# Kernel optimization log

Measured on AMD Instinct MI355X. Metric: run time of the kernel, lower is better.

## Reference

```python
import jax, jax.numpy as jnp
import numpy as np

H = 16          # head_count
D = 1024        # model_dim
DH = D // H     # dim_per_head


def setup_inputs() -> dict:
    key = jax.random.key(0)
    ks = jax.random.split(key, 12)
    B, S = 4, 2048
    s = 1.0 / np.sqrt(D)
    return {
        "key": jax.random.normal(ks[0], (B, S, D), jnp.float32),
        "value": jax.random.normal(ks[1], (B, S, D), jnp.float32),
        "query": jax.random.normal(ks[2], (B, S, D), jnp.float32),
        "Wk": jax.random.normal(ks[3], (D, D), jnp.float32) * s,
        "bk": jax.random.normal(ks[4], (D,), jnp.float32) * 0.01,
        "Wv": jax.random.normal(ks[5], (D, D), jnp.float32) * s,
        "bv": jax.random.normal(ks[6], (D,), jnp.float32) * 0.01,
        "Wq": jax.random.normal(ks[7], (D, D), jnp.float32) * s,
        "bq": jax.random.normal(ks[8], (D,), jnp.float32) * 0.01,
        "Wo": jax.random.normal(ks[9], (D, D), jnp.float32) * s,
        "bo": jax.random.normal(ks[10], (D,), jnp.float32) * 0.01,
    }


def _split_heads(x):
    # [B, S, D] -> [B, H, S, DH]
    B, S, _ = x.shape
    return x.reshape(B, S, H, DH).transpose(0, 2, 1, 3)


def reference(key, value, query, Wk, bk, Wv, bv, Wq, bq, Wo, bo):
    B, Sq, _ = query.shape
    Sk = key.shape[1]
    k_up = _split_heads(key @ Wk + bk)      # [B,H,Sk,DH]
    v_up = _split_heads(value @ Wv + bv)    # [B,H,Sk,DH]
    q_up = _split_heads(query @ Wq + bq) / jnp.sqrt(jnp.asarray(DH, query.dtype))
    scores = jnp.einsum('bhqd,bhkd->bhqk', q_up, k_up)  # [B,H,Sq,Sk]
    attn = jax.nn.softmax(scores, axis=-1)
    # dropout p=0.0 -> identity
    ctx = jnp.einsum('bhqk,bhkd->bhqd', attn, v_up)      # [B,H,Sq,DH]
    ctx = ctx.transpose(0, 2, 1, 3).reshape(B, Sq, D)    # combine heads
    output = ctx @ Wo + bo
    top_attn = attn[:, 0, :, :]
    return output, top_attn
```

## Files before the change

kernel.cpp:

```cpp
#include <hip/hip_runtime.h>
#include <stdint.h>

typedef __bf16 bf16_t;
typedef __bf16 bf16x8 __attribute__((ext_vector_type(8)));
typedef float f32x4 __attribute__((ext_vector_type(4)));
typedef uint32_t u32x4 __attribute__((ext_vector_type(4)));

#define D_MODEL 1024
#define NH      16
#define DH      64
#define SEQ     2048
#define BATCH   4
#define MROWS   (BATCH * SEQ)

#define VCOL(d, c) ((c) ^ ((((d) >> 3) & 3) << 4))

__device__ __forceinline__ void gll16(const void* g, void* l) {
    __builtin_amdgcn_global_load_lds(
        (const __attribute__((address_space(1))) void*)g,
        (__attribute__((address_space(3))) void*)l, 16, 0, 0);
}

__global__ void transpose_w(const float* __restrict__ W0, const float* __restrict__ W1,
                            const float* __restrict__ W2, const float* __restrict__ W3,
                            bf16_t* __restrict__ out) {
    __shared__ bf16_t tile[32][33];
    const int z = blockIdx.z;
    const float* src = (z == 0) ? W0 : (z == 1) ? W1 : (z == 2) ? W2 : W3;
    bf16_t* dst = out + (size_t)z * (D_MODEL * D_MODEL);
    const int bx = blockIdx.x * 32, by = blockIdx.y * 32;
    const int tx = threadIdx.x, ty = threadIdx.y;
#pragma unroll
    for (int i = 0; i < 4; ++i)
        tile[ty + i * 8][tx] = (bf16_t)src[(size_t)(by + ty + i * 8) * D_MODEL + bx + tx];
    __syncthreads();
#pragma unroll
    for (int i = 0; i < 4; ++i)
        dst[(size_t)(bx + ty + i * 8) * D_MODEL + by + tx] = tile[tx][ty + i * 8];
}

__global__ __launch_bounds__(256) void cast_bf16(const float* __restrict__ in,
                                                 bf16_t* __restrict__ out, int n8) {
    const int i = blockIdx.x * 256 + threadIdx.x;
    if (i < n8) {
        const float4 x = ((const float4*)in)[i * 2];
        const float4 y = ((const float4*)in)[i * 2 + 1];
        bf16x8 t;
        t[0] = (bf16_t)x.x; t[1] = (bf16_t)x.y; t[2] = (bf16_t)x.z; t[3] = (bf16_t)x.w;
        t[4] = (bf16_t)y.x; t[5] = (bf16_t)y.y; t[6] = (bf16_t)y.z; t[7] = (bf16_t)y.w;
        ((bf16x8*)out)[i] = t;
    }
}

template<int OUT_MODE>
__global__ __launch_bounds__(256) void proj_gemm(const bf16_t* __restrict__ A,
                                                 const bf16_t* __restrict__ Wt,
                                                 const float* __restrict__ bias,
                                                 void* __restrict__ C_,
                                                 float scale) {
    __shared__ __align__(16) bf16_t As[128 * 32];
    __shared__ __align__(16) bf16_t Bs[128 * 32];
    const int tid  = threadIdx.x;
    const int lane = tid & 63;
    const int w    = tid >> 6;
    const int wrow = (w >> 1) * 64;
    const int wcol = (w & 1) * 64;
    const int m0 = blockIdx.y * 128;
    const int n0 = blockIdx.x * 128;
    const int l15  = lane & 15;
    const int quad = lane >> 4;
    const int srow = w * 32 + (lane >> 2);
    const int scol = (lane & 3) * 8;

    f32x4 acc[4][4];
#pragma unroll
    for (int i = 0; i < 4; ++i)
#pragma unroll
        for (int j = 0; j < 4; ++j)
#pragma unroll
            for (int r = 0; r < 4; ++r) acc[i][j][r] = 0.0f;

    for (int kt = 0; kt < 32; ++kt) {
        const int k0 = kt * 32;
#pragma unroll
        for (int j = 0; j < 2; ++j) {
            gll16(A  + (size_t)(m0 + srow + j * 16) * D_MODEL + k0 + scol,
                  &As[(w * 32 + j * 16) * 32]);
            gll16(Wt + (size_t)(n0 + srow + j * 16) * D_MODEL + k0 + scol,
                  &Bs[(w * 32 + j * 16) * 32]);
        }
        __syncthreads();
        bf16x8 af[4], bf[4];
#pragma unroll
        for (int mi = 0; mi < 4; ++mi)
            af[mi] = *(const bf16x8*)&As[(wrow + mi * 16 + l15) * 32 + quad * 8];
#pragma unroll
        for (int ni = 0; ni < 4; ++ni)
            bf[ni] = *(const bf16x8*)&Bs[(wcol + ni * 16 + l15) * 32 + quad * 8];
#pragma unroll
        for (int mi = 0; mi < 4; ++mi)
#pragma unroll
            for (int ni = 0; ni < 4; ++ni)
                acc[mi][ni] = __builtin_amdgcn_mfma_f32_16x16x32_bf16(af[mi], bf[ni], acc[mi][ni], 0, 0, 0);
        __syncthreads();
    }

#pragma unroll
    for (int ni = 0; ni < 4; ++ni) {
        const int col = n0 + wcol + ni * 16 + l15;
        const float bc = bias[col];
#pragma unroll
        for (int mi = 0; mi < 4; ++mi) {
#pragma unroll
            for (int r = 0; r < 4; ++r) {
                const int row = m0 + wrow + mi * 16 + quad * 4 + r;
                const float v = (acc[mi][ni][r] + bc) * scale;
                if (OUT_MODE == 1) {
                    ((float*)C_)[(size_t)row * D_MODEL + col] = v;
                } else if (OUT_MODE == 0) {
                    ((bf16_t*)C_)[(size_t)row * D_MODEL + col] = (bf16_t)v;
                } else {
                    const int bb = row >> 11, ss = row & 2047;
                    const int hh = col >> 6,  dd = col & 63;
                    ((bf16_t*)C_)[((size_t)(bb * 16 + hh) * 64 + dd) * 2048 + ss] = (bf16_t)v;
                }
            }
        }
    }
}

__device__ __forceinline__ uint32_t pk2(float a, float b) {
    union { bf16_t h[2]; uint32_t u; } x;
    x.h[0] = (bf16_t)a; x.h[1] = (bf16_t)b;
    return x.u;
}

__global__ __launch_bounds__(256) void flash_attn(const bf16_t* __restrict__ Qu,
                                                  const bf16_t* __restrict__ Ku,
                                                  const bf16_t* __restrict__ Vt_g,
                                                  bf16_t* __restrict__ ctx) {
    const int qt = blockIdx.x;
    const int bh = blockIdx.y;
    const int b = bh >> 4, h = bh & 15;
    const int tid  = threadIdx.x;
    const int lane = tid & 63;
    const int w    = tid >> 6;
    const int l15  = lane & 15;
    const int quad = lane >> 4;

    __shared__ __align__(16) bf16_t Ks[64][72];
    __shared__ __align__(16) bf16_t Vs[64][72];

    const size_t base_qk = (size_t)b * SEQ * D_MODEL + (size_t)h * DH;
    const size_t base_v  = (size_t)bh * DH * SEQ;
    const int qrow0 = qt * 64 + w * 16;

    bf16x8 qf[2];
#pragma unroll
    for (int ks = 0; ks < 2; ++ks)
        qf[ks] = *(const bf16x8*)(Qu + base_qk + (size_t)(qrow0 + l15) * D_MODEL + ks * 32 + quad * 8);

    const int srow = tid >> 2;
    const int sc0  = (tid & 3) * 16;
    const bf16_t* kg = Ku   + base_qk + (size_t)srow * D_MODEL + sc0;
    const bf16_t* vg = Vt_g + base_v  + (size_t)srow * SEQ + sc0;

    bf16x8 kp0, kp1, vp0, vp1;
#define LOAD_TILE(KB)                                                    \
    do {                                                                 \
        kp0 = *(const bf16x8*)(kg + (size_t)(KB) * D_MODEL);             \
        kp1 = *(const bf16x8*)(kg + (size_t)(KB) * D_MODEL + 8);         \
        vp0 = *(const bf16x8*)(vg + (KB));                               \
        vp1 = *(const bf16x8*)(vg + (KB) + 8);                           \
    } while (0)
#define WRITE_TILE()                                                     \
    do {                                                                 \
        *(bf16x8*)&Ks[srow][VCOL(srow, sc0)]     = kp0;                  \
        *(bf16x8*)&Ks[srow][VCOL(srow, sc0 + 8)] = kp1;                  \
        *(bf16x8*)&Vs[srow][VCOL(srow, sc0)]     = vp0;                  \
        *(bf16x8*)&Vs[srow][VCOL(srow, sc0 + 8)] = vp1;                  \
    } while (0)

    float m_q = -__builtin_inff();
    float l_q = 0.0f;
    f32x4 cacc[4];
#pragma unroll
    for (int ds = 0; ds < 4; ++ds)
#pragma unroll
        for (int r = 0; r < 4; ++r) cacc[ds][r] = 0.0f;

    LOAD_TILE(0);
    WRITE_TILE();

    for (int kt = 0; kt < 32; ++kt) {
        __syncthreads();
        if (kt + 1 < 32) LOAD_TILE((kt + 1) * 64);

        f32x4 s[4];
#pragma unroll
        for (int ki = 0; ki < 4; ++ki)
#pragma unroll
            for (int r = 0; r < 4; ++r) s[ki][r] = 0.0f;
#pragma unroll
        for (int ks = 0; ks < 2; ++ks)
#pragma unroll
            for (int ki = 0; ki < 4; ++ki) {
                const int kr = ki * 16 + l15;
                bf16x8 kf = *(const bf16x8*)&Ks[kr][VCOL(kr, ks * 32 + quad * 8)];
                s[ki] = __builtin_amdgcn_mfma_f32_16x16x32_bf16(kf, qf[ks], s[ki], 0, 0, 0);
            }

        float v = s[0][0];
#pragma unroll
        for (int ki = 0; ki < 4; ++ki)
#pragma unroll
            for (int r = 0; r < 4; ++r) v = fmaxf(v, s[ki][r]);
        v = fmaxf(v, __shfl_xor(v, 16));
        v = fmaxf(v, __shfl_xor(v, 32));
        const float mn  = fmaxf(m_q, v);
        const float alq = __expf(m_q - mn);
        m_q = mn;

        float t = 0.0f;
        uint32_t pk_[4][2];
#pragma unroll
        for (int ki = 0; ki < 4; ++ki) {
            const float p0 = __expf(s[ki][0] - mn);
            const float p1 = __expf(s[ki][1] - mn);
            const float p2 = __expf(s[ki][2] - mn);
            const float p3 = __expf(s[ki][3] - mn);
            t += (p0 + p1) + (p2 + p3);
            pk_[ki][0] = pk2(p0, p1);
            pk_[ki][1] = pk2(p2, p3);
        }
        t += __shfl_xor(t, 16);
        t += __shfl_xor(t, 32);
        l_q = l_q * alq + t;

        float al_c[4];
#pragma unroll
        for (int r = 0; r < 4; ++r) al_c[r] = __shfl(alq, quad * 4 + r, 16);
#pragma unroll
        for (int ds = 0; ds < 4; ++ds)
#pragma unroll
            for (int r = 0; r < 4; ++r) cacc[ds][r] *= al_c[r];

        const int srcA = l15 + ((quad & 1) << 5);
        const bool hi  = (quad & 2) != 0;
        bf16x8 af[2];
#pragma unroll
        for (int ks = 0; ks < 2; ++ks) {
            const uint32_t a0 = pk_[2 * ks][0],     a1 = pk_[2 * ks][1];
            const uint32_t b0 = pk_[2 * ks + 1][0], b1 = pk_[2 * ks + 1][1];
            union { u32x4 d; bf16x8 v8; } cv;
            const uint32_t xa = (uint32_t)__shfl((int)a0, srcA);
            const uint32_t xb = (uint32_t)__shfl((int)b0, srcA);
            cv.d.x = hi ? xb : xa;
            const uint32_t ya = (uint32_t)__shfl((int)a1, srcA);
            const uint32_t yb = (uint32_t)__shfl((int)b1, srcA);
            cv.d.y = hi ? yb : ya;
            const uint32_t za = (uint32_t)__shfl((int)a0, srcA + 16);
            const uint32_t zb = (uint32_t)__shfl((int)b0, srcA + 16);
            cv.d.z = hi ? zb : za;
            const uint32_t wa = (uint32_t)__shfl((int)a1, srcA + 16);
            const uint32_t wb = (uint32_t)__shfl((int)b1, srcA + 16);
            cv.d.w = hi ? wb : wa;
            af[ks] = cv.v8;
        }

#pragma unroll
        for (int ks = 0; ks < 2; ++ks)
#pragma unroll
            for (int ds = 0; ds < 4; ++ds) {
                const int vr = ds * 16 + l15;
                bf16x8 vf = *(const bf16x8*)&Vs[vr][VCOL(vr, ks * 32 + quad * 8)];
                cacc[ds] = __builtin_amdgcn_mfma_f32_16x16x32_bf16(af[ks], vf, cacc[ds], 0, 0, 0);
            }

        __syncthreads();
        if (kt + 1 < 32) WRITE_TILE();
    }

    float l_c[4];
#pragma unroll
    for (int r = 0; r < 4; ++r) l_c[r] = __shfl(l_q, quad * 4 + r, 16);
#pragma unroll
    for (int r = 0; r < 4; ++r) {
        const float rl = 1.0f / l_c[r];
        const int q = qrow0 + quad * 4 + r;
#pragma unroll
        for (int ds = 0; ds < 4; ++ds)
            ctx[(size_t)(b * SEQ + q) * D_MODEL + h * DH + ds * 16 + l15] = (bf16_t)(cacc[ds][r] * rl);
    }
#undef LOAD_TILE
#undef WRITE_TILE
}

__global__ __launch_bounds__(256) void attn_h0(const bf16_t* __restrict__ Qu,
                                               const bf16_t* __restrict__ Ku,
                                               float* __restrict__ out) {
    const int qt = blockIdx.x;
    const int b  = blockIdx.y;
    const int tid  = threadIdx.x;
    const int lane = tid & 63;
    const int w    = tid >> 6;
    const int l15  = lane & 15;
    const int quad = lane >> 4;

    const size_t base_b = (size_t)b * SEQ * D_MODEL;
    const int qrow0 = qt * 64 + w * 16;

    bf16x8 qf[2];
#pragma unroll
    for (int ks = 0; ks < 2; ++ks)
        qf[ks] = *(const bf16x8*)(Qu + base_b + (size_t)(qrow0 + l15) * D_MODEL + ks * 32 + quad * 8);

    float m_r[4], l_r[4];
#pragma unroll
    for (int r = 0; r < 4; ++r) { m_r[r] = -__builtin_inff(); l_r[r] = 0.0f; }

    for (int kt = 0; kt < 32; ++kt) {
        const int kb = kt * 64;
        f32x4 s[4];
#pragma unroll
        for (int ki = 0; ki < 4; ++ki)
#pragma unroll
            for (int r = 0; r < 4; ++r) s[ki][r] = 0.0f;
#pragma unroll
        for (int ks = 0; ks < 2; ++ks)
#pragma unroll
            for (int ki = 0; ki < 4; ++ki) {
                bf16x8 kf = *(const bf16x8*)(Ku + base_b + (size_t)(kb + ki * 16 + l15) * D_MODEL + ks * 32 + quad * 8);
                s[ki] = __builtin_amdgcn_mfma_f32_16x16x32_bf16(qf[ks], kf, s[ki], 0, 0, 0);
            }
#pragma unroll
        for (int r = 0; r < 4; ++r) {
            float v = fmaxf(fmaxf(s[0][r], s[1][r]), fmaxf(s[2][r], s[3][r]));
#pragma unroll
            for (int off = 1; off < 16; off <<= 1) v = fmaxf(v, __shfl_xor(v, off, 16));
            const float mn = fmaxf(m_r[r], v);
            const float al = __expf(m_r[r] - mn);
            m_r[r] = mn;
            float t = __expf(s[0][r] - mn) + __expf(s[1][r] - mn)
                    + __expf(s[2][r] - mn) + __expf(s[3][r] - mn);
#pragma unroll
            for (int off = 1; off < 16; off <<= 1) t += __shfl_xor(t, off, 16);
            l_r[r] = l_r[r] * al + t;
        }
    }
    float rl[4];
#pragma unroll
    for (int r = 0; r < 4; ++r) rl[r] = 1.0f / l_r[r];

    for (int kt = 0; kt < 32; ++kt) {
        const int kb = kt * 64;
        f32x4 s[4];
#pragma unroll
        for (int ki = 0; ki < 4; ++ki)
#pragma unroll
            for (int r = 0; r < 4; ++r) s[ki][r] = 0.0f;
#pragma unroll
        for (int ks = 0; ks < 2; ++ks)
#pragma unroll
            for (int ki = 0; ki < 4; ++ki) {
                bf16x8 kf = *(const bf16x8*)(Ku + base_b + (size_t)(kb + ki * 16 + l15) * D_MODEL + ks * 32 + quad * 8);
                s[ki] = __builtin_amdgcn_mfma_f32_16x16x32_bf16(qf[ks], kf, s[ki], 0, 0, 0);
            }
#pragma unroll
        for (int ki = 0; ki < 4; ++ki)
#pragma unroll
            for (int r = 0; r < 4; ++r) {
                const int q = qrow0 + quad * 4 + r;
                out[(size_t)(b * SEQ + q) * SEQ + kb + ki * 16 + l15] =
                    __expf(s[ki][r] - m_r[r]) * rl[r];
            }
    }
}

extern "C" void kernel_launch(void* const* d_in, const int* in_sizes, int n_in,
                              void* d_out, int out_size, void* d_ws, size_t ws_size,
                              hipStream_t stream) {
    const float* key   = (const float*)d_in[0];
    const float* value = (const float*)d_in[1];
    const float* query = (const float*)d_in[2];
    const float* Wk = (const float*)d_in[3];
    const float* bk = (const float*)d_in[4];
    const float* Wv = (const float*)d_in[5];
    const float* bv = (const float*)d_in[6];
    const float* Wq = (const float*)d_in[7];
    const float* bq = (const float*)d_in[8];
    const float* Wo = (const float*)d_in[9];
    const float* bo = (const float*)d_in[10];

    float* out_proj = (float*)d_out;
    float* out_attn = (float*)d_out + (size_t)MROWS * D_MODEL;

    char* ws = (char*)d_ws;
    bf16_t* Wt  = (bf16_t*)ws;
    bf16_t* Kup = (bf16_t*)(ws + (size_t) 8 * 1024 * 1024);
    bf16_t* Qup = (bf16_t*)(ws + (size_t)24 * 1024 * 1024);

    bf16_t* Vt_g = (bf16_t*)out_attn;
    bf16_t* ctx  = Vt_g + (size_t)MROWS * D_MODEL;
    bf16_t* C1   = (bf16_t*)((char*)out_attn + ((size_t)32 << 20));
    bf16_t* C2   = (bf16_t*)((char*)out_attn + ((size_t)48 << 20));

    const bf16_t* Wt_k = Wt;
    const bf16_t* Wt_v = Wt + 1 * D_MODEL * D_MODEL;
    const bf16_t* Wt_q = Wt + 2 * D_MODEL * D_MODEL;
    const bf16_t* Wt_o = Wt + 3 * D_MODEL * D_MODEL;

    const int n8 = MROWS * D_MODEL / 8;

    transpose_w<<<dim3(32, 32, 4), dim3(32, 8), 0, stream>>>(Wk, Wv, Wq, Wo, Wt);

    cast_bf16<<<dim3(4096), 256, 0, stream>>>(key,   C1, n8);
    cast_bf16<<<dim3(4096), 256, 0, stream>>>(value, C2, n8);

    proj_gemm<0><<<dim3(8, 64), 256, 0, stream>>>(C1, Wt_k, bk, Kup,  1.0f);
    cast_bf16<<<dim3(4096), 256, 0, stream>>>(query, C1, n8);
    proj_gemm<2><<<dim3(8, 64), 256, 0, stream>>>(C2, Wt_v, bv, Vt_g, 1.0f);
    proj_gemm<0><<<dim3(8, 64), 256, 0, stream>>>(C1, Wt_q, bq, Qup,  0.125f);

    flash_attn<<<dim3(32, 64), 256, 0, stream>>>(Qup, Kup, Vt_g, ctx);

    proj_gemm<1><<<dim3(8, 64), 256, 0, stream>>>(ctx, Wt_o, bo, out_proj, 1.0f);

    attn_h0<<<dim3(32, 4), 256, 0, stream>>>(Qup, Kup, out_attn);
}
```

Before: 584.3 us.

## Reuse flash softmax stats for head-0 attention, exp2 with lazy rescale, fused casts

flash_attn now writes the per-row max and inverse sum for head 0 to a workspace buffer. attn_h0 becomes a single-pass kernel tiled over key blocks (4096 blocks instead of 128), so it no longer recomputes the softmax statistics in a serial two-pass loop. The softmax uses a raw v_exp_f32 with log2e folded into the Q projection scale. Rescaling of the accumulator is skipped unless the running max grows by more than 8, which saves ALU work at a small accuracy cost. The three input casts are merged into one launch by giving the query its own buffer.

New measurement: 520.3 us. -11.0%, faster.

```diff
diff --git a/kernel.cpp b/kernel.cpp
--- a/kernel.cpp
+++ b/kernel.cpp
@@ -12,6 +12,10 @@
 #define SEQ     2048
 #define BATCH   4
 #define MROWS   (BATCH * SEQ)
+
+__device__ __forceinline__ float ex2(float x) {
+    float r; asm("v_exp_f32 %0, %1" : "=v"(r) : "v"(x)); return r;
+}
 
 #define VCOL(d, c) ((c) ^ ((((d) >> 3) & 3) << 4))
 
@@ -39,9 +43,16 @@
         dst[(size_t)(bx + ty + i * 8) * D_MODEL + by + tx] = tile[tx][ty + i * 8];
 }
 
-__global__ __launch_bounds__(256) void cast_bf16(const float* __restrict__ in,
-                                                 bf16_t* __restrict__ out, int n8) {
+__global__ __launch_bounds__(256) void cast3_bf16(const float* __restrict__ i0,
+                                                  const float* __restrict__ i1,
+                                                  const float* __restrict__ i2,
+                                                  bf16_t* __restrict__ o0,
+                                                  bf16_t* __restrict__ o1,
+                                                  bf16_t* __restrict__ o2, int n8) {
     const int i = blockIdx.x * 256 + threadIdx.x;
+    const int z = blockIdx.y;
+    const float* in  = (z == 0) ? i0 : (z == 1) ? i1 : i2;
+    bf16_t*      out = (z == 0) ? o0 : (z == 1) ? o1 : o2;
     if (i < n8) {
         const float4 x = ((const float4*)in)[i * 2];
         const float4 y = ((const float4*)in)[i * 2 + 1];
@@ -138,7 +149,9 @@
 __global__ __launch_bounds__(256) void flash_attn(const bf16_t* __restrict__ Qu,
                                                   const bf16_t* __restrict__ Ku,
                                                   const bf16_t* __restrict__ Vt_g,
-                                                  bf16_t* __restrict__ ctx) {
+                                                  bf16_t* __restrict__ ctx,
+                                                  float* __restrict__ Mb,
+                                                  float* __restrict__ Lb) {
     const int qt = blockIdx.x;
     const int bh = blockIdx.y;
     const int b = bh >> 4, h = bh & 15;
@@ -217,33 +230,36 @@
             for (int r = 0; r < 4; ++r) v = fmaxf(v, s[ki][r]);
         v = fmaxf(v, __shfl_xor(v, 16));
         v = fmaxf(v, __shfl_xor(v, 32));
-        const float mn  = fmaxf(m_q, v);
-        const float alq = __expf(m_q - mn);
-        m_q = mn;
+
+        if (!__all(v <= m_q + 8.0f)) {
+            const float mn  = fmaxf(m_q, v);
+            const float alq = ex2(m_q - mn);
+            m_q = mn;
+            l_q *= alq;
+            float al_c[4];
+#pragma unroll
+            for (int r = 0; r < 4; ++r) al_c[r] = __shfl(alq, quad * 4 + r, 16);
+#pragma unroll
+            for (int ds = 0; ds < 4; ++ds)
+#pragma unroll
+                for (int r = 0; r < 4; ++r) cacc[ds][r] *= al_c[r];
+        }
 
         float t = 0.0f;
         uint32_t pk_[4][2];
 #pragma unroll
         for (int ki = 0; ki < 4; ++ki) {
-            const float p0 = __expf(s[ki][0] - mn);
-            const float p1 = __expf(s[ki][1] - mn);
-            const float p2 = __expf(s[ki][2] - mn);
-            const float p3 = __expf(s[ki][3] - mn);
+            const float p0 = ex2(s[ki][0] - m_q);
+            const float p1 = ex2(s[ki][1] - m_q);
+            const float p2 = ex2(s[ki][2] - m_q);
+            const float p3 = ex2(s[ki][3] - m_q);
             t += (p0 + p1) + (p2 + p3);
             pk_[ki][0] = pk2(p0, p1);
             pk_[ki][1] = pk2(p2, p3);
         }
         t += __shfl_xor(t, 16);
         t += __shfl_xor(t, 32);
-        l_q = l_q * alq + t;
-
-        float al_c[4];
-#pragma unroll
-        for (int r = 0; r < 4; ++r) al_c[r] = __shfl(alq, quad * 4 + r, 16);
-#pragma unroll
-        for (int ds = 0; ds < 4; ++ds)
-#pragma unroll
-            for (int r = 0; r < 4; ++r) cacc[ds][r] *= al_c[r];
+        l_q += t;
 
         const int srcA = l15 + ((quad & 1) << 5);
         const bool hi  = (quad & 2) != 0;
@@ -281,6 +297,12 @@
         if (kt + 1 < 32) WRITE_TILE();
     }
 
+    if (h == 0 && quad == 0) {
+        const int q = b * SEQ + qrow0 + l15;
+        Mb[q] = m_q;
+        Lb[q] = 1.0f / l_q;
+    }
+
     float l_c[4];
 #pragma unroll
     for (int r = 0; r < 4; ++r) l_c[r] = __shfl(l_q, quad * 4 + r, 16);
@@ -298,9 +320,12 @@
 
 __global__ __launch_bounds__(256) void attn_h0(const bf16_t* __restrict__ Qu,
                                                const bf16_t* __restrict__ Ku,
+                                               const float* __restrict__ Mb,
+                                               const float* __restrict__ Lb,
                                                float* __restrict__ out) {
     const int qt = blockIdx.x;
-    const int b  = blockIdx.y;
+    const int ktile = blockIdx.y;
+    const int b  = blockIdx.z;
     const int tid  = threadIdx.x;
     const int lane = tid & 63;
     const int w    = tid >> 6;
@@ -309,72 +334,41 @@
 
     const size_t base_b = (size_t)b * SEQ * D_MODEL;
     const int qrow0 = qt * 64 + w * 16;
+    const int kb = ktile * 64;
 
     bf16x8 qf[2];
 #pragma unroll
     for (int ks = 0; ks < 2; ++ks)
         qf[ks] = *(const bf16x8*)(Qu + base_b + (size_t)(qrow0 + l15) * D_MODEL + ks * 32 + quad * 8);
 
-    float m_r[4], l_r[4];
-#pragma unroll
-    for (int r = 0; r < 4; ++r) { m_r[r] = -__builtin_inff(); l_r[r] = 0.0f; }
-
-    for (int kt = 0; kt < 32; ++kt) {
-        const int kb = kt * 64;
-        f32x4 s[4];
-#pragma unroll
-        for (int ki = 0; ki < 4; ++ki)
-#pragma unroll
-            for (int r = 0; r < 4; ++r) s[ki][r] = 0.0f;
-#pragma unroll
-        for (int ks = 0; ks < 2; ++ks)
-#pragma unroll
-            for (int ki = 0; ki < 4; ++ki) {
-                bf16x8 kf = *(const bf16x8*)(Ku + base_b + (size_t)(kb + ki * 16 + l15) * D_MODEL + ks * 32 + quad * 8);
-                s[ki] = __builtin_amdgcn_mfma_f32_16x16x32_bf16(qf[ks], kf, s[ki], 0, 0, 0);
-            }
+    f32x4 s[4];
+#pragma unroll
+    for (int ki = 0; ki < 4; ++ki)
+#pragma unroll
+        for (int r = 0; r < 4; ++r) s[ki][r] = 0.0f;
+#pragma unroll
+    for (int ks = 0; ks < 2; ++ks)
+#pragma unroll
+        for (int ki = 0; ki < 4; ++ki) {
+            bf16x8 kf = *(const bf16x8*)(Ku + base_b + (size_t)(kb + ki * 16 + l15) * D_MODEL + ks * 32 + quad * 8);
+            s[ki] = __builtin_amdgcn_mfma_f32_16x16x32_bf16(qf[ks], kf, s[ki], 0, 0, 0);
+        }
+
+    float m_v[4], rl_v[4];
+#pragma unroll
+    for (int r = 0; r < 4; ++r) {
+        const int q = b * SEQ + qrow0 + quad * 4 + r;
+        m_v[r]  = Mb[q];
+        rl_v[r] = Lb[q];
+    }
+#pragma unroll
+    for (int ki = 0; ki < 4; ++ki)
 #pragma unroll
         for (int r = 0; r < 4; ++r) {
-            float v = fmaxf(fmaxf(s[0][r], s[1][r]), fmaxf(s[2][r], s[3][r]));
-#pragma unroll
-            for (int off = 1; off < 16; off <<= 1) v = fmaxf(v, __shfl_xor(v, off, 16));
-            const float mn = fmaxf(m_r[r], v);
-            const float al = __expf(m_r[r] - mn);
-            m_r[r] = mn;
-            float t = __expf(s[0][r] - mn) + __expf(s[1][r] - mn)
-                    + __expf(s[2][r] - mn) + __expf(s[3][r] - mn);
-#pragma unroll
-            for (int off = 1; off < 16; off <<= 1) t += __shfl_xor(t, off, 16);
-            l_r[r] = l_r[r] * al + t;
-        }
-    }
-    float rl[4];
-#pragma unroll
-    for (int r = 0; r < 4; ++r) rl[r] = 1.0f / l_r[r];
-
-    for (int kt = 0; kt < 32; ++kt) {
-        const int kb = kt * 64;
-        f32x4 s[4];
-#pragma unroll
-        for (int ki = 0; ki < 4; ++ki)
-#pragma unroll
-            for (int r = 0; r < 4; ++r) s[ki][r] = 0.0f;
-#pragma unroll
-        for (int ks = 0; ks < 2; ++ks)
-#pragma unroll
-            for (int ki = 0; ki < 4; ++ki) {
-                bf16x8 kf = *(const bf16x8*)(Ku + base_b + (size_t)(kb + ki * 16 + l15) * D_MODEL + ks * 32 + quad * 8);
-                s[ki] = __builtin_amdgcn_mfma_f32_16x16x32_bf16(qf[ks], kf, s[ki], 0, 0, 0);
-            }
-#pragma unroll
-        for (int ki = 0; ki < 4; ++ki)
-#pragma unroll
-            for (int r = 0; r < 4; ++r) {
-                const int q = qrow0 + quad * 4 + r;
-                out[(size_t)(b * SEQ + q) * SEQ + kb + ki * 16 + l15] =
-                    __expf(s[ki][r] - m_r[r]) * rl[r];
-            }
-    }
+            const int q = qrow0 + quad * 4 + r;
+            out[(size_t)(b * SEQ + q) * SEQ + kb + ki * 16 + l15] =
+                ex2(s[ki][r] - m_v[r]) * rl_v[r];
+        }
 }
 
 extern "C" void kernel_launch(void* const* d_in, const int* in_sizes, int n_in,
@@ -399,9 +393,12 @@
     bf16_t* Wt  = (bf16_t*)ws;
     bf16_t* Kup = (bf16_t*)(ws + (size_t) 8 * 1024 * 1024);
     bf16_t* Qup = (bf16_t*)(ws + (size_t)24 * 1024 * 1024);
+    float*  Mb  = (float*)ws;
+    float*  Lb  = Mb + MROWS;
 
     bf16_t* Vt_g = (bf16_t*)out_attn;
-    bf16_t* ctx  = Vt_g + (size_t)MROWS * D_MODEL;
+    bf16_t* Cq   = Vt_g + (size_t)MROWS * D_MODEL;
+    bf16_t* ctx  = Cq;
     bf16_t* C1   = (bf16_t*)((char*)out_attn + ((size_t)32 << 20));
     bf16_t* C2   = (bf16_t*)((char*)out_attn + ((size_t)48 << 20));
 
@@ -414,17 +411,16 @@
 
     transpose_w<<<dim3(32, 32, 4), dim3(32, 8), 0, stream>>>(Wk, Wv, Wq, Wo, Wt);
 
-    cast_bf16<<<dim3(4096), 256, 0, stream>>>(key,   C1, n8);
-    cast_bf16<<<dim3(4096), 256, 0, stream>>>(value, C2, n8);
+    cast3_bf16<<<dim3(4096, 3), 256, 0, stream>>>(key, value, query, C1, C2, Cq, n8);
 
     proj_gemm<0><<<dim3(8, 64), 256, 0, stream>>>(C1, Wt_k, bk, Kup,  1.0f);
-    cast_bf16<<<dim3(4096), 256, 0, stream>>>(query, C1, n8);
     proj_gemm<2><<<dim3(8, 64), 256, 0, stream>>>(C2, Wt_v, bv, Vt_g, 1.0f);
-    proj_gemm<0><<<dim3(8, 64), 256, 0, stream>>>(C1, Wt_q, bq, Qup,  0.125f);
-
-    flash_attn<<<dim3(32, 64), 256, 0, stream>>>(Qup, Kup, Vt_g, ctx);
+    proj_gemm<0><<<dim3(8, 64), 256, 0, stream>>>(Cq, Wt_q, bq, Qup,
+                                                  0.125f * 1.4426950408889634f);
+
+    flash_attn<<<dim3(32, 64), 256, 0, stream>>>(Qup, Kup, Vt_g, ctx, Mb, Lb);
 
     proj_gemm<1><<<dim3(8, 64), 256, 0, stream>>>(ctx, Wt_o, bo, out_proj, 1.0f);
 
-    attn_h0<<<dim3(32, 4), 256, 0, stream>>>(Qup, Kup, out_attn);
-}
+    attn_h0<<<dim3(32, 32, 4), 256, 0, stream>>>(Qup, Kup, Mb, Lb, out_attn);
+}
```
